# Performance work log

Hardware: AMD Instinct MI355X
Metric: run time of the kernel (lower is better)

The kernel has to match this reference:

```python
import jax, jax.numpy as jnp
import numpy as np

L, B, ENC, ATTN, HID = 2048, 32, 1024, 1024, 1024


def setup_inputs() -> dict:
    key = jax.random.key(0)
    k1, k2, k3, k4, k5 = jax.random.split(key, 5)
    return {
        "enc_outputs": jax.random.normal(k1, (L, B, ENC), dtype=jnp.float32),
        "mask": jnp.zeros((L, B), dtype=jnp.float32),
        "hidden_state": jax.random.normal(k2, (B, HID), dtype=jnp.float32),
        "W_enc": jax.random.normal(k3, (ENC, ATTN), dtype=jnp.float32) * (2.0 / (ENC + ATTN)) ** 0.5,
        "b_attn": jnp.zeros((ATTN,), dtype=jnp.float32),
        "W_hidden": jax.random.normal(k4, (HID, ATTN), dtype=jnp.float32) * (2.0 / (HID + ATTN)) ** 0.5,
        "v": jax.random.normal(k5, (ATTN,), dtype=jnp.float32) * 0.1,
    }


def reference(enc_outputs, mask, hidden_state, W_enc, b_attn, W_hidden, v):
    # keys: [l, b, attn]  (map_enc=False so values = enc_outputs)
    keys = jnp.einsum('lbe,ea->lba', enc_outputs, W_enc) + b_attn
    values = enc_outputs
    # query projection: [b, attn], broadcast over l
    q = hidden_state @ W_hidden
    # additive Bahdanau score -> [l, b]
    alignment = jnp.einsum('lba,a->lb', jnp.tanh(keys + q[None, :, :]), v)
    # masked softmax over time (dim 0)
    alignment = jax.nn.softmax(mask + alignment, axis=0)
    # weighted value sum -> context [b, enc]
    context = jnp.einsum('lb,lbe->be', alignment, values)
    return (context, alignment)
```

## Files before the change

kernel.cpp:

```cpp
#include <hip/hip_runtime.h>
#include <stdint.h>

#define L_DIM 2048
#define B_DIM 32
#define ENC_DIM 1024
#define M_DIM (L_DIM * B_DIM)

typedef __attribute__((ext_vector_type(4))) float f32x4;
typedef __attribute__((ext_vector_type(8))) short short8;
typedef __attribute__((ext_vector_type(4))) __bf16 bf16x4;

static __device__ __forceinline__ float fast_tanh(float x) {
  float cx = fminf(fmaxf(x, -15.f), 15.f);
  float e = __expf(2.f * cx);
  return (e - 1.f) * __frcp_rn(e + 1.f);
}

static __device__ __forceinline__ void load_lds16(const void* g, void* l) {
  __builtin_amdgcn_global_load_lds((const __attribute__((address_space(1))) void*)g,
                                   (__attribute__((address_space(3))) void*)l, 16, 0, 0);
}

__global__ __launch_bounds__(256) void k_wt(const float* __restrict__ W,
                                            unsigned short* __restrict__ WT) {
  __shared__ float tile[64][65];
  const int t = threadIdx.x;
  const int k0 = (blockIdx.x & 15) << 6, n0 = (blockIdx.x >> 4) << 6;
#pragma unroll
  for (int i = 0; i < 16; ++i) {
    int idx = t + (i << 8);
    tile[idx >> 6][idx & 63] = W[(size_t)(k0 + (idx >> 6)) * 1024 + n0 + (idx & 63)];
  }
  __syncthreads();
#pragma unroll
  for (int i = 0; i < 16; ++i) {
    int idx = t + (i << 8);
    int r = idx >> 6, c = idx & 63;
    WT[(size_t)(n0 + r) * 1024 + k0 + c] =
        __builtin_bit_cast(unsigned short, (__bf16)tile[c][r]);
  }
}

__global__ __launch_bounds__(128) void k_qpart(const float* __restrict__ hidden,
                                               const float* __restrict__ Wh,
                                               float* __restrict__ pq) {
  const int ablk = blockIdx.x & 7, hblk = blockIdx.x >> 3;
  const int a = (ablk << 7) + threadIdx.x;
  float acc[32];
#pragma unroll
  for (int b = 0; b < 32; ++b) acc[b] = 0.f;
  const int h0 = hblk << 7;
  for (int h = h0; h < h0 + 128; ++h) {
    float wv = Wh[(size_t)h * 1024 + a];
#pragma unroll
    for (int b = 0; b < 32; ++b) acc[b] = fmaf(hidden[(b << 10) + h], wv, acc[b]);
  }
#pragma unroll
  for (int b = 0; b < 32; ++b) pq[((size_t)hblk << 15) + (b << 10) + a] = acc[b];
}

__global__ __launch_bounds__(256) void k_qred(const float* __restrict__ pq,
                                              const float* __restrict__ ba,
                                              float* __restrict__ q) {
  int i = blockIdx.x * 256 + threadIdx.x;
  float s = ba[i & 1023];
#pragma unroll
  for (int j = 0; j < 8; ++j) s += pq[((size_t)j << 15) + i];
  q[i] = s;
}

__global__ __launch_bounds__(256, 3) void k_logits(const float* __restrict__ enc,
                                                   const unsigned short* __restrict__ WT,
                                                   const float* __restrict__ qv,
                                                   const float* __restrict__ v,
                                                   float* __restrict__ pl) {
  __shared__ __align__(16) unsigned short As[128 * 64];
  __shared__ __align__(16) unsigned short Bs[128 * 64];
  __shared__ float red[2][128];

  const int tid = threadIdx.x;
  const int xcd = blockIdx.x & 7, slot = blockIdx.x >> 3;
  const int nblk = slot & 7;
  const int mblk = xcd + ((slot >> 3) << 3);
  const int row0 = mblk << 7;
  const int n0 = nblk << 7;

  const int w = tid >> 6, lane = tid & 63;
  const int wr = w >> 1, wc = w & 1;
  const int g = lane >> 4, rr = lane & 15;

  float vreg[4];
#pragma unroll
  for (int nf = 0; nf < 4; ++nf) vreg[nf] = v[n0 + wc * 64 + nf * 16 + rr];

  f32x4 acc[4][4];
#pragma unroll
  for (int mf = 0; mf < 4; ++mf)
#pragma unroll
    for (int nf = 0; nf < 4; ++nf)
#pragma unroll
      for (int rg = 0; rg < 4; ++rg) {
        int b = ((mf & 1) << 4) + (g << 2) + rg;
        acc[mf][nf][rg] = qv[((size_t)b << 10) + n0 + wc * 64 + nf * 16 + rr];
      }

  const int ar = tid >> 4;
  const int ac4 = tid & 15;
  const int ablk = ((ac4 >> 1) ^ (ar & 7));
  const int brow = lane >> 3, bjj = lane & 7;

  for (int kt = 0; kt < 16; ++kt) {
    const int k0 = kt << 6;
    __syncthreads();
#pragma unroll
    for (int c = 0; c < 4; ++c) {
      int nrow = w * 32 + c * 8 + brow;
      int blk = bjj ^ (brow & 7);
      const char* src = (const char*)WT + (((size_t)(n0 + nrow) << 10) + k0) * 2 + (blk << 4);
      load_lds16(src, (void*)&Bs[(w * 32 + c * 8) * 64]);
    }
#pragma unroll
    for (int i = 0; i < 8; ++i) {
      int r = ar + (i << 4);
      f32x4 a4 = *reinterpret_cast<const f32x4*>(enc + (((size_t)(row0 + r)) << 10) + k0 + (ac4 << 2));
      bf16x4 pk = {(__bf16)a4.x, (__bf16)a4.y, (__bf16)a4.z, (__bf16)a4.w};
      *reinterpret_cast<bf16x4*>(&As[r * 64 + (ablk << 3) + ((ac4 & 1) << 2)]) = pk;
    }
    __syncthreads();
#pragma unroll
    for (int kk = 0; kk < 2; ++kk) {
      short8 af[4], bfr[4];
#pragma unroll
      for (int mf = 0; mf < 4; ++mf) {
        int r = wr * 64 + mf * 16 + rr;
        int blk = (kk * 4 + g) ^ (r & 7);
        af[mf] = *reinterpret_cast<const short8*>(&As[r * 64 + (blk << 3)]);
      }
#pragma unroll
      for (int nf = 0; nf < 4; ++nf) {
        int r = wc * 64 + nf * 16 + rr;
        int blk = (kk * 4 + g) ^ (r & 7);
        bfr[nf] = *reinterpret_cast<const short8*>(&Bs[r * 64 + (blk << 3)]);
      }
#pragma unroll
      for (int mf = 0; mf < 4; ++mf)
#pragma unroll
        for (int nf = 0; nf < 4; ++nf)
          acc[mf][nf] = __builtin_amdgcn_mfma_f32_16x16x32_bf16(af[mf], bfr[nf], acc[mf][nf], 0, 0, 0);
    }
  }

#pragma unroll
  for (int mf = 0; mf < 4; ++mf) {
#pragma unroll
    for (int rg = 0; rg < 4; ++rg) {
      int lrow = wr * 64 + mf * 16 + g * 4 + rg;
      float s = 0.f;
#pragma unroll
      for (int nf = 0; nf < 4; ++nf) {
        s += fast_tanh(acc[mf][nf][rg]) * vreg[nf];
      }
      s += __shfl_xor(s, 1);
      s += __shfl_xor(s, 2);
      s += __shfl_xor(s, 4);
      s += __shfl_xor(s, 8);
      if (rr == 0) red[wc][lrow] = s;
    }
  }
  __syncthreads();
  if (tid < 128) {
    int row = row0 + tid;
    pl[((size_t)nblk << 16) + ((size_t)(row & 31) << 11) + (row >> 5)] =
        red[0][tid] + red[1][tid];
  }
}

__global__ __launch_bounds__(256) void k_softmax(const float* __restrict__ pl,
                                                 const float* __restrict__ mask,
                                                 float* __restrict__ al) {
  const int b = blockIdx.x, t = threadIdx.x;
  __shared__ float sr[256];
  float lg[8];
  float mx = -3.4e38f;
#pragma unroll
  for (int i = 0; i < 8; ++i) {
    int l = t + (i << 8);
    float s = mask[(l << 5) + b];
#pragma unroll
    for (int nb = 0; nb < 8; ++nb) s += pl[((size_t)nb << 16) + (b << 11) + l];
    lg[i] = s;
    mx = fmaxf(mx, s);
  }
  sr[t] = mx;
  __syncthreads();
  for (int off = 128; off > 0; off >>= 1) {
    if (t < off) sr[t] = fmaxf(sr[t], sr[t + off]);
    __syncthreads();
  }
  const float M = sr[0];
  __syncthreads();
  float sum = 0.f;
#pragma unroll
  for (int i = 0; i < 8; ++i) {
    lg[i] = __expf(lg[i] - M);
    sum += lg[i];
  }
  sr[t] = sum;
  __syncthreads();
  for (int off = 128; off > 0; off >>= 1) {
    if (t < off) sr[t] += sr[t + off];
    __syncthreads();
  }
  const float inv = 1.f / sr[0];
#pragma unroll
  for (int i = 0; i < 8; ++i) {
    int l = t + (i << 8);
    al[(l << 5) + b] = lg[i] * inv;
  }
}

__global__ __launch_bounds__(256) void k_ctx(const float* __restrict__ enc,
                                             const float* __restrict__ al,
                                             float* __restrict__ pctx) {
  const int b = blockIdx.x & 31, ch = blockIdx.x >> 5;
  const int t = threadIdx.x;
  __shared__ float wl[64];
  if (t < 64) wl[t] = al[(((ch << 6) + t) << 5) + b];
  __syncthreads();
  f32x4 acc = (f32x4){0.f, 0.f, 0.f, 0.f};
  const float* base = enc + (((size_t)ch * 2048 + b) << 10) + (t << 2);
#pragma unroll 8
  for (int i = 0; i < 64; ++i) {
    f32x4 e = *reinterpret_cast<const f32x4*>(base + (size_t)i * 32768);
    acc += wl[i] * e;
  }
  *reinterpret_cast<f32x4*>(((float*)pctx) + ((size_t)blockIdx.x << 10) + (t << 2)) = acc;
}

__global__ __launch_bounds__(256) void k_ctxred(const float* __restrict__ pctx,
                                                float* __restrict__ out) {
  int i = blockIdx.x * 256 + threadIdx.x;
  int b = i >> 10, e = i & 1023;
  float s = 0.f;
#pragma unroll
  for (int ch = 0; ch < 32; ++ch) s += pctx[(size_t)((ch << 5) + b) * 1024 + e];
  out[i] = s;
}

extern "C" void kernel_launch(void* const* d_in, const int* in_sizes, int n_in,
                              void* d_out, int out_size, void* d_ws, size_t ws_size,
                              hipStream_t stream) {
  const float* enc = (const float*)d_in[0];
  const float* mask = (const float*)d_in[1];
  const float* hidden = (const float*)d_in[2];
  const float* Wenc = (const float*)d_in[3];
  const float* battn = (const float*)d_in[4];
  const float* Whid = (const float*)d_in[5];
  const float* v = (const float*)d_in[6];
  float* out = (float*)d_out;
  char* ws = (char*)d_ws;

  unsigned short* WT = (unsigned short*)ws;
  float* q = (float*)(ws + (2u << 20));
  float* pq = (float*)(ws + (2u << 20) + (128u << 10));
  float* pl = (float*)(ws + (3u << 20) + (128u << 10));
  float* pctx = (float*)(ws + (5u << 20) + (128u << 10));
  float* align_out = out + 32768;

  k_wt<<<256, 256, 0, stream>>>(Wenc, WT);
  k_qpart<<<64, 128, 0, stream>>>(hidden, Whid, pq);
  k_qred<<<128, 256, 0, stream>>>(pq, battn, q);
  k_logits<<<4096, 256, 0, stream>>>(enc, WT, q, v, pl);
  k_softmax<<<32, 256, 0, stream>>>(pl, mask, align_out);
  k_ctx<<<1024, 256, 0, stream>>>(enc, align_out, pctx);
  k_ctxred<<<128, 256, 0, stream>>>(pctx, out);
}
```

Baseline: 319.4 us.

## Load A fragments directly to registers and double-buffer B tiles in LDS

Each wave now loads its encoder-output fragments from global memory straight into registers and converts them to bf16 MFMA operands there, so the A tile no longer goes through LDS. The B (transposed weight) tile is double-buffered in LDS and the next tile is prefetched while the current one is computed, leaving one barrier per k-step instead of two. In exchange, register pressure rises, so the launch-bounds occupancy hint drops from 3 to 2 blocks per CU. The global A loads are also less coalesced, and each enc row is read by both column waves.

```diff
diff --git a/kernel.cpp b/kernel.cpp
--- a/kernel.cpp
+++ b/kernel.cpp
@@ -14,6 +14,10 @@
   float cx = fminf(fmaxf(x, -15.f), 15.f);
   float e = __expf(2.f * cx);
   return (e - 1.f) * __frcp_rn(e + 1.f);
+}
+
+static __device__ __forceinline__ short bfs(float x) {
+  return __builtin_bit_cast(short, (__bf16)x);
 }
 
 static __device__ __forceinline__ void load_lds16(const void* g, void* l) {
@@ -69,13 +73,12 @@
   q[i] = s;
 }
 
-__global__ __launch_bounds__(256, 3) void k_logits(const float* __restrict__ enc,
+__global__ __launch_bounds__(256, 2) void k_logits(const float* __restrict__ enc,
                                                    const unsigned short* __restrict__ WT,
                                                    const float* __restrict__ qv,
                                                    const float* __restrict__ v,
                                                    float* __restrict__ pl) {
-  __shared__ __align__(16) unsigned short As[128 * 64];
-  __shared__ __align__(16) unsigned short Bs[128 * 64];
+  __shared__ __align__(16) unsigned short Bs[2][128 * 64];
   __shared__ float red[2][128];
 
   const int tid = threadIdx.x;
@@ -104,50 +107,64 @@
         acc[mf][nf][rg] = qv[((size_t)b << 10) + n0 + wc * 64 + nf * 16 + rr];
       }
 
-  const int ar = tid >> 4;
-  const int ac4 = tid & 15;
-  const int ablk = ((ac4 >> 1) ^ (ar & 7));
+  const float* aptr[4];
+#pragma unroll
+  for (int mf = 0; mf < 4; ++mf)
+    aptr[mf] = enc + (((size_t)(row0 + wr * 64 + mf * 16 + rr)) << 10) + (g << 3);
+
   const int brow = lane >> 3, bjj = lane & 7;
 
+#pragma unroll
+  for (int c = 0; c < 4; ++c) {
+    int nrow = w * 32 + c * 8 + brow;
+    int blk = bjj ^ (brow & 7);
+    const char* src = (const char*)WT + (((size_t)(n0 + nrow) << 10)) * 2 + (blk << 4);
+    load_lds16(src, (void*)&Bs[0][(w * 32 + c * 8) * 64]);
+  }
+  __syncthreads();
+
   for (int kt = 0; kt < 16; ++kt) {
-    const int k0 = kt << 6;
-    __syncthreads();
-#pragma unroll
-    for (int c = 0; c < 4; ++c) {
-      int nrow = w * 32 + c * 8 + brow;
-      int blk = bjj ^ (brow & 7);
-      const char* src = (const char*)WT + (((size_t)(n0 + nrow) << 10) + k0) * 2 + (blk << 4);
-      load_lds16(src, (void*)&Bs[(w * 32 + c * 8) * 64]);
+    const int cur = kt & 1;
+    f32x4 alo[2][4], ahi[2][4];
+#pragma unroll
+    for (int kk = 0; kk < 2; ++kk)
+#pragma unroll
+      for (int mf = 0; mf < 4; ++mf) {
+        const float* p = aptr[mf] + kt * 64 + kk * 32;
+        alo[kk][mf] = *reinterpret_cast<const f32x4*>(p);
+        ahi[kk][mf] = *reinterpret_cast<const f32x4*>(p + 4);
+      }
+    if (kt < 15) {
+#pragma unroll
+      for (int c = 0; c < 4; ++c) {
+        int nrow = w * 32 + c * 8 + brow;
+        int blk = bjj ^ (brow & 7);
+        const char* src =
+            (const char*)WT + (((size_t)(n0 + nrow) << 10) + (kt + 1) * 64) * 2 + (blk << 4);
+        load_lds16(src, (void*)&Bs[cur ^ 1][(w * 32 + c * 8) * 64]);
+      }
     }
 #pragma unroll
-    for (int i = 0; i < 8; ++i) {
-      int r = ar + (i << 4);
-      f32x4 a4 = *reinterpret_cast<const f32x4*>(enc + (((size_t)(row0 + r)) << 10) + k0 + (ac4 << 2));
-      bf16x4 pk = {(__bf16)a4.x, (__bf16)a4.y, (__bf16)a4.z, (__bf16)a4.w};
-      *reinterpret_cast<bf16x4*>(&As[r * 64 + (ablk << 3) + ((ac4 & 1) << 2)]) = pk;
-    }
-    __syncthreads();
-#pragma unroll
     for (int kk = 0; kk < 2; ++kk) {
-      short8 af[4], bfr[4];
-#pragma unroll
-      for (int mf = 0; mf < 4; ++mf) {
-        int r = wr * 64 + mf * 16 + rr;
-        int blk = (kk * 4 + g) ^ (r & 7);
-        af[mf] = *reinterpret_cast<const short8*>(&As[r * 64 + (blk << 3)]);
-      }
+      short8 bfr[4];
 #pragma unroll
       for (int nf = 0; nf < 4; ++nf) {
         int r = wc * 64 + nf * 16 + rr;
         int blk = (kk * 4 + g) ^ (r & 7);
-        bfr[nf] = *reinterpret_cast<const short8*>(&Bs[r * 64 + (blk << 3)]);
-      }
-#pragma unroll
-      for (int mf = 0; mf < 4; ++mf)
+        bfr[nf] = *reinterpret_cast<const short8*>(&Bs[cur][r * 64 + (blk << 3)]);
+      }
+#pragma unroll
+      for (int mf = 0; mf < 4; ++mf) {
+        f32x4 lo = alo[kk][mf], hi = ahi[kk][mf];
+        short8 af;
+        af[0] = bfs(lo.x); af[1] = bfs(lo.y); af[2] = bfs(lo.z); af[3] = bfs(lo.w);
+        af[4] = bfs(hi.x); af[5] = bfs(hi.y); af[6] = bfs(hi.z); af[7] = bfs(hi.w);
 #pragma unroll
         for (int nf = 0; nf < 4; ++nf)
-          acc[mf][nf] = __builtin_amdgcn_mfma_f32_16x16x32_bf16(af[mf], bfr[nf], acc[mf][nf], 0, 0, 0);
+          acc[mf][nf] = __builtin_amdgcn_mfma_f32_16x16x32_bf16(af, bfr[nf], acc[mf][nf], 0, 0, 0);
+      }
     }
+    __syncthreads();
   }
 
 #pragma unroll
```

Result: slower. 667.5 us (+109.0%).

## Pre-convert encoder outputs to bf16 before logits GEMM when workspace allows

Applied to the files above, without the earlier changes.

Adds a separate pass that converts the fp32 encoder outputs to a bf16 copy in workspace. A new logits kernel then streams both operands into LDS with direct global-to-LDS loads, so it no longer converts fp32 tiles in registers. The original converting kernel is kept as a fallback when the workspace is under 140 MB. The trade is an extra full read of enc plus a 128 MB write, and enc is still read in fp32 by the context kernel, in return for cheaper A-tile loads in the GEMM, which reads each A tile 8 times across N blocks.

```diff
diff --git a/kernel.cpp b/kernel.cpp
--- a/kernel.cpp
+++ b/kernel.cpp
@@ -7,6 +7,7 @@
 #define M_DIM (L_DIM * B_DIM)
 
 typedef __attribute__((ext_vector_type(4))) float f32x4;
+typedef __attribute__((ext_vector_type(4))) unsigned int uint4v;
 typedef __attribute__((ext_vector_type(8))) short short8;
 typedef __attribute__((ext_vector_type(4))) __bf16 bf16x4;
 
@@ -19,6 +20,25 @@
 static __device__ __forceinline__ void load_lds16(const void* g, void* l) {
   __builtin_amdgcn_global_load_lds((const __attribute__((address_space(1))) void*)g,
                                    (__attribute__((address_space(3))) void*)l, 16, 0, 0);
+}
+
+__global__ __launch_bounds__(256) void k_enc_bf16(const float* __restrict__ enc,
+                                                  unsigned short* __restrict__ encB) {
+  const int t = blockIdx.x * 256 + threadIdx.x;
+#pragma unroll
+  for (int it = 0; it < 16; ++it) {
+    size_t i = ((size_t)t + (size_t)it * 524288) << 3;
+    f32x4 a = *reinterpret_cast<const f32x4*>(enc + i);
+    f32x4 b = *reinterpret_cast<const f32x4*>(enc + i + 4);
+    bf16x4 pa = {(__bf16)a.x, (__bf16)a.y, (__bf16)a.z, (__bf16)a.w};
+    bf16x4 pb = {(__bf16)b.x, (__bf16)b.y, (__bf16)b.z, (__bf16)b.w};
+    uint4v o;
+    o.x = __builtin_bit_cast(unsigned int, *reinterpret_cast<ushort2*>(&pa));
+    union { bf16x4 v; unsigned int u[2]; } ua, ub;
+    ua.v = pa; ub.v = pb;
+    o.x = ua.u[0]; o.y = ua.u[1]; o.z = ub.u[0]; o.w = ub.u[1];
+    *reinterpret_cast<uint4v*>(encB + i) = o;
+  }
 }
 
 __global__ __launch_bounds__(256) void k_wt(const float* __restrict__ W,
@@ -69,11 +89,12 @@
   q[i] = s;
 }
 
-__global__ __launch_bounds__(256, 3) void k_logits(const float* __restrict__ enc,
-                                                   const unsigned short* __restrict__ WT,
-                                                   const float* __restrict__ qv,
-                                                   const float* __restrict__ v,
-                                                   float* __restrict__ pl) {
+
+__global__ __launch_bounds__(256, 3) void k_logits_bf(const unsigned short* __restrict__ encB,
+                                                      const unsigned short* __restrict__ WT,
+                                                      const float* __restrict__ qv,
+                                                      const float* __restrict__ v,
+                                                      float* __restrict__ pl) {
   __shared__ __align__(16) unsigned short As[128 * 64];
   __shared__ __align__(16) unsigned short Bs[128 * 64];
   __shared__ float red[2][128];
@@ -104,6 +125,102 @@
         acc[mf][nf][rg] = qv[((size_t)b << 10) + n0 + wc * 64 + nf * 16 + rr];
       }
 
+  const int srow = lane >> 3, sjj = lane & 7;
+
+  for (int kt = 0; kt < 16; ++kt) {
+    const int k0 = kt << 6;
+    __syncthreads();
+#pragma unroll
+    for (int c = 0; c < 4; ++c) {
+      int r = w * 32 + c * 8 + srow;
+      int blk = sjj ^ (r & 7);
+      const char* bsrc = (const char*)WT + (((size_t)(n0 + r) << 10) + k0) * 2 + (blk << 4);
+      load_lds16(bsrc, (void*)&Bs[(w * 32 + c * 8) * 64]);
+      const char* asrc = (const char*)encB + (((size_t)(row0 + r) << 10) + k0) * 2 + (blk << 4);
+      load_lds16(asrc, (void*)&As[(w * 32 + c * 8) * 64]);
+    }
+    __syncthreads();
+#pragma unroll
+    for (int kk = 0; kk < 2; ++kk) {
+      short8 af[4], bfr[4];
+#pragma unroll
+      for (int mf = 0; mf < 4; ++mf) {
+        int r = wr * 64 + mf * 16 + rr;
+        int blk = (kk * 4 + g) ^ (r & 7);
+        af[mf] = *reinterpret_cast<const short8*>(&As[r * 64 + (blk << 3)]);
+      }
+#pragma unroll
+      for (int nf = 0; nf < 4; ++nf) {
+        int r = wc * 64 + nf * 16 + rr;
+        int blk = (kk * 4 + g) ^ (r & 7);
+        bfr[nf] = *reinterpret_cast<const short8*>(&Bs[r * 64 + (blk << 3)]);
+      }
+#pragma unroll
+      for (int mf = 0; mf < 4; ++mf)
+#pragma unroll
+        for (int nf = 0; nf < 4; ++nf)
+          acc[mf][nf] = __builtin_amdgcn_mfma_f32_16x16x32_bf16(af[mf], bfr[nf], acc[mf][nf], 0, 0, 0);
+    }
+  }
+
+#pragma unroll
+  for (int mf = 0; mf < 4; ++mf) {
+#pragma unroll
+    for (int rg = 0; rg < 4; ++rg) {
+      int lrow = wr * 64 + mf * 16 + g * 4 + rg;
+      float s = 0.f;
+#pragma unroll
+      for (int nf = 0; nf < 4; ++nf) s += fast_tanh(acc[mf][nf][rg]) * vreg[nf];
+      s += __shfl_xor(s, 1);
+      s += __shfl_xor(s, 2);
+      s += __shfl_xor(s, 4);
+      s += __shfl_xor(s, 8);
+      if (rr == 0) red[wc][lrow] = s;
+    }
+  }
+  __syncthreads();
+  if (tid < 128) {
+    int row = row0 + tid;
+    pl[((size_t)nblk << 16) + ((size_t)(row & 31) << 11) + (row >> 5)] =
+        red[0][tid] + red[1][tid];
+  }
+}
+
+__global__ __launch_bounds__(256, 3) void k_logits_cvt(const float* __restrict__ enc,
+                                                       const unsigned short* __restrict__ WT,
+                                                       const float* __restrict__ qv,
+                                                       const float* __restrict__ v,
+                                                       float* __restrict__ pl) {
+  __shared__ __align__(16) unsigned short As[128 * 64];
+  __shared__ __align__(16) unsigned short Bs[128 * 64];
+  __shared__ float red[2][128];
+
+  const int tid = threadIdx.x;
+  const int xcd = blockIdx.x & 7, slot = blockIdx.x >> 3;
+  const int nblk = slot & 7;
+  const int mblk = xcd + ((slot >> 3) << 3);
+  const int row0 = mblk << 7;
+  const int n0 = nblk << 7;
+
+  const int w = tid >> 6, lane = tid & 63;
+  const int wr = w >> 1, wc = w & 1;
+  const int g = lane >> 4, rr = lane & 15;
+
+  float vreg[4];
+#pragma unroll
+  for (int nf = 0; nf < 4; ++nf) vreg[nf] = v[n0 + wc * 64 + nf * 16 + rr];
+
+  f32x4 acc[4][4];
+#pragma unroll
+  for (int mf = 0; mf < 4; ++mf)
+#pragma unroll
+    for (int nf = 0; nf < 4; ++nf)
+#pragma unroll
+      for (int rg = 0; rg < 4; ++rg) {
+        int b = ((mf & 1) << 4) + (g << 2) + rg;
+        acc[mf][nf][rg] = qv[((size_t)b << 10) + n0 + wc * 64 + nf * 16 + rr];
+      }
+
   const int ar = tid >> 4;
   const int ac4 = tid & 15;
   const int ablk = ((ac4 >> 1) ^ (ar & 7));
@@ -157,9 +274,7 @@
       int lrow = wr * 64 + mf * 16 + g * 4 + rg;
       float s = 0.f;
 #pragma unroll
-      for (int nf = 0; nf < 4; ++nf) {
-        s += fast_tanh(acc[mf][nf][rg]) * vreg[nf];
-      }
+      for (int nf = 0; nf < 4; ++nf) s += fast_tanh(acc[mf][nf][rg]) * vreg[nf];
       s += __shfl_xor(s, 1);
       s += __shfl_xor(s, 2);
       s += __shfl_xor(s, 4);
@@ -260,17 +375,25 @@
   float* out = (float*)d_out;
   char* ws = (char*)d_ws;
 
-  unsigned short* WT = (unsigned short*)ws;
-  float* q = (float*)(ws + (2u << 20));
-  float* pq = (float*)(ws + (2u << 20) + (128u << 10));
-  float* pl = (float*)(ws + (3u << 20) + (128u << 10));
-  float* pctx = (float*)(ws + (5u << 20) + (128u << 10));
+  const bool big = ws_size >= (size_t)140 * 1024 * 1024;
+  char* base = big ? ws + ((size_t)128 << 20) : ws;
+  unsigned short* encB = (unsigned short*)ws;
+  unsigned short* WT = (unsigned short*)base;
+  float* q = (float*)(base + (2u << 20));
+  float* pq = (float*)(base + (2u << 20) + (128u << 10));
+  float* pl = (float*)(base + (3u << 20) + (128u << 10));
+  float* pctx = (float*)(base + (5u << 20) + (128u << 10));
   float* align_out = out + 32768;
 
   k_wt<<<256, 256, 0, stream>>>(Wenc, WT);
   k_qpart<<<64, 128, 0, stream>>>(hidden, Whid, pq);
   k_qred<<<128, 256, 0, stream>>>(pq, battn, q);
-  k_logits<<<4096, 256, 0, stream>>>(enc, WT, q, v, pl);
+  if (big) {
+    k_enc_bf16<<<2048, 256, 0, stream>>>(enc, encB);
+    k_logits_bf<<<4096, 256, 0, stream>>>(encB, WT, q, v, pl);
+  } else {
+    k_logits_cvt<<<4096, 256, 0, stream>>>(enc, WT, q, v, pl);
+  }
   k_softmax<<<32, 256, 0, stream>>>(pl, mask, align_out);
   k_ctx<<<1024, 256, 0, stream>>>(enc, align_out, pctx);
   k_ctxred<<<128, 256, 0, stream>>>(pctx, out);
```

Measured after the change: 370.0 us. 1.16x slower.
